# Optimization experiments

Measured on AMD Instinct MI355X. Metric: run time of the kernel, lower is better.

## Reference

```python
import jax, jax.numpy as jnp
import numpy as np

V, E, B, NODES_PER_GRAPH = 100000, 128, 4096, 64
N = B * NODES_PER_GRAPH  # 262144 nodes per side
EPS = 1e-6


def setup_inputs() -> dict:
    key = jax.random.key(0)
    k1, k2, k3, k4, k5, k6 = jax.random.split(key, 6)
    left_x = jax.random.randint(k1, (N, 1), 0, V, dtype=jnp.int64 if jax.config.jax_enable_x64 else jnp.int32)
    right_x = jax.random.randint(k2, (N, 1), 0, V, dtype=left_x.dtype)
    # sorted segment ids with every graph non-empty (64 nodes per graph)
    batch_ids = jnp.repeat(jnp.arange(B, dtype=left_x.dtype), NODES_PER_GRAPH)
    label = jax.random.randint(k3, (B,), 0, 2).astype(jnp.float32)
    emb_table = jax.random.normal(k4, (V, E), dtype=jnp.float32)
    W = jax.random.normal(k5, (E, E), dtype=jnp.float32) / np.sqrt(E)
    b = jax.random.normal(k6, (E,), dtype=jnp.float32) * 0.01
    return {
        "left_x": left_x,
        "left_graph_index": jnp.arange(B, dtype=left_x.dtype),
        "right_x": right_x,
        "right_graph_index": jnp.arange(B, dtype=left_x.dtype),
        "left_x_batch": batch_ids,
        "right_x_batch": batch_ids,
        "label": label,
        "emb_table": emb_table,
        "W": W,
        "b": b,
    }


def _side_emb(x, x_batch, emb_table, W, b, num_segments):
    node_emb = emb_table[x[:, 0]]                       # [N, E] gather
    pooled = jax.ops.segment_max(node_emb, x_batch,      # [B, E] scatter-max
                                 num_segments=num_segments,
                                 indices_are_sorted=True)
    return pooled @ W.T + b                              # trans_linear


def reference(left_x, left_graph_index, right_x, right_graph_index,
              left_x_batch, right_x_batch, label, emb_table, W, b):
    num_segments = label.shape[0]
    left_final = _side_emb(left_x, left_x_batch, emb_table, W, b, num_segments)
    right_final = _side_emb(right_x, right_x_batch, emb_table, W, b, num_segments)
    # torch CosineSimilarity(eps=1e-6): clamp each norm at eps
    dot = jnp.sum(left_final * right_final, axis=-1)
    nl = jnp.maximum(jnp.linalg.norm(left_final, axis=-1), EPS)
    nr = jnp.maximum(jnp.linalg.norm(right_final, axis=-1), EPS)
    cos = dot / (nl * nr)                                # [B]
    # ContrastiveLoss(margin=1.0), size_average=True
    losses = 0.5 * ((1.0 - label) * cos ** 2
                    + label * jnp.maximum(1.0 - cos, 0.0) ** 2)
    sim_loss = losses.mean()
    return sim_loss, cos
```

## Files before the change

kernel.cpp:

```cpp
#include <hip/hip_runtime.h>
#include <math.h>

#define B_GRAPHS 4096
#define NPG 64
#define E_DIM 128
#define INV_B (1.0f / 4096.0f)

static __device__ __forceinline__ float4 fmax4(float4 a, float4 b) {
    return make_float4(fmaxf(a.x, b.x), fmaxf(a.y, b.y),
                       fmaxf(a.z, b.z), fmaxf(a.w, b.w));
}

__global__ __launch_bounds__(256, 6) void fused_graph_sim_k(
    const int* __restrict__ lx, const int* __restrict__ rx,
    const float* __restrict__ emb, const float* __restrict__ W,
    const float* __restrict__ bias, const float* __restrict__ label,
    float* __restrict__ out)
{
    const int g    = blockIdx.x;
    const int t    = threadIdx.x;
    const int w    = t >> 6;
    const int lane = t & 63;

    __shared__ int   idxL[NPG], idxR[NPG];
    __shared__ float red[2][4][E_DIM];
    __shared__ float4 P4[2][32];
    __shared__ float wred[3][4];

    if (t < NPG)          idxL[t]       = lx[g * NPG + t];
    else if (t < 2 * NPG) idxR[t - NPG] = rx[g * NPG + (t - NPG)];
    __syncthreads();

    const int n0 = t >> 5;
    const int q  = t & 31;

    const float4* __restrict__ e4 = reinterpret_cast<const float4*>(emb);
    float4 l0 = e4[(size_t)idxL[     n0] * 32 + q];
    float4 l1 = e4[(size_t)idxL[ 8 + n0] * 32 + q];
    float4 l2 = e4[(size_t)idxL[16 + n0] * 32 + q];
    float4 l3 = e4[(size_t)idxL[24 + n0] * 32 + q];
    float4 l4 = e4[(size_t)idxL[32 + n0] * 32 + q];
    float4 l5 = e4[(size_t)idxL[40 + n0] * 32 + q];
    float4 l6 = e4[(size_t)idxL[48 + n0] * 32 + q];
    float4 l7 = e4[(size_t)idxL[56 + n0] * 32 + q];
    float4 r0 = e4[(size_t)idxR[     n0] * 32 + q];
    float4 r1 = e4[(size_t)idxR[ 8 + n0] * 32 + q];
    float4 r2 = e4[(size_t)idxR[16 + n0] * 32 + q];
    float4 r3 = e4[(size_t)idxR[24 + n0] * 32 + q];
    float4 r4 = e4[(size_t)idxR[32 + n0] * 32 + q];
    float4 r5 = e4[(size_t)idxR[40 + n0] * 32 + q];
    float4 r6 = e4[(size_t)idxR[48 + n0] * 32 + q];
    float4 r7 = e4[(size_t)idxR[56 + n0] * 32 + q];

    float4 aL = fmax4(fmax4(fmax4(l0, l1), fmax4(l2, l3)),
                      fmax4(fmax4(l4, l5), fmax4(l6, l7)));
    float4 aR = fmax4(fmax4(fmax4(r0, r1), fmax4(r2, r3)),
                      fmax4(fmax4(r4, r5), fmax4(r6, r7)));

    aL.x = fmaxf(aL.x, __shfl_xor(aL.x, 32));
    aL.y = fmaxf(aL.y, __shfl_xor(aL.y, 32));
    aL.z = fmaxf(aL.z, __shfl_xor(aL.z, 32));
    aL.w = fmaxf(aL.w, __shfl_xor(aL.w, 32));
    aR.x = fmaxf(aR.x, __shfl_xor(aR.x, 32));
    aR.y = fmaxf(aR.y, __shfl_xor(aR.y, 32));
    aR.z = fmaxf(aR.z, __shfl_xor(aR.z, 32));
    aR.w = fmaxf(aR.w, __shfl_xor(aR.w, 32));

    if (lane < 32) {
        const int o = w * 32 + lane;
        red[0][0][o] = aL.x; red[0][1][o] = aL.y;
        red[0][2][o] = aL.z; red[0][3][o] = aL.w;
        red[1][0][o] = aR.x; red[1][1][o] = aR.y;
        red[1][2][o] = aR.z; red[1][3][o] = aR.w;
    }
    __syncthreads();

    if (t < 64) {
        const int side = t >> 5;
        const int qq   = t & 31;
        float4 m;
        m.x = fmaxf(fmaxf(red[side][0][qq],      red[side][0][32 + qq]),
                    fmaxf(red[side][0][64 + qq], red[side][0][96 + qq]));
        m.y = fmaxf(fmaxf(red[side][1][qq],      red[side][1][32 + qq]),
                    fmaxf(red[side][1][64 + qq], red[side][1][96 + qq]));
        m.z = fmaxf(fmaxf(red[side][2][qq],      red[side][2][32 + qq]),
                    fmaxf(red[side][2][64 + qq], red[side][2][96 + qq]));
        m.w = fmaxf(fmaxf(red[side][3][qq],      red[side][3][32 + qq]),
                    fmaxf(red[side][3][64 + qq], red[side][3][96 + qq]));
        P4[side][qq] = m;
    }
    __syncthreads();

    float acc;
    {
        const int side = t & 1;
        const int e    = t >> 1;
        acc = bias[e];
        const float4* __restrict__ wr =
            reinterpret_cast<const float4*>(W) + (size_t)e * 32;
        const float4* __restrict__ pv = P4[side];
        #pragma unroll 8
        for (int fi = 0; fi < 32; ++fi) {
            const float4 wv = wr[fi];
            const float4 p  = pv[fi];
            acc = fmaf(p.x, wv.x, acc);
            acc = fmaf(p.y, wv.y, acc);
            acc = fmaf(p.z, wv.z, acc);
            acc = fmaf(p.w, wv.w, acc);
        }
    }

    {
        const float other = __shfl_xor(acc, 1);
        const float l = (t & 1) ? other : acc;
        const float r = (t & 1) ? acc   : other;
        float dot = l * r;
        float nl  = l * l;
        float nr  = r * r;
        #pragma unroll
        for (int off = 1; off < 64; off <<= 1) {
            dot += __shfl_xor(dot, off);
            nl  += __shfl_xor(nl,  off);
            nr  += __shfl_xor(nr,  off);
        }
        if (lane == 0) {
            wred[0][w] = dot; wred[1][w] = nl; wred[2][w] = nr;
        }
    }
    __syncthreads();

    if (t == 0) {
        const float dd = 0.5f * (wred[0][0] + wred[0][1] + wred[0][2] + wred[0][3]);
        const float ll = 0.5f * (wred[1][0] + wred[1][1] + wred[1][2] + wred[1][3]);
        const float rr = 0.5f * (wred[2][0] + wred[2][1] + wred[2][2] + wred[2][3]);
        const float nlv = fmaxf(sqrtf(ll), 1e-6f);
        const float nrv = fmaxf(sqrtf(rr), 1e-6f);
        const float c   = dd / (nlv * nrv);
        out[1 + g] = c;
        const float lab = label[g];
        const float mm  = fmaxf(1.0f - c, 0.0f);
        const float loss = 0.5f * ((1.0f - lab) * c * c + lab * mm * mm);
        atomicAdd(out, loss * INV_B);
    }
}

extern "C" void kernel_launch(void* const* d_in, const int* in_sizes, int n_in,
                              void* d_out, int out_size, void* d_ws, size_t ws_size,
                              hipStream_t stream)
{
    const int*   lx    = (const int*)d_in[0];
    const int*   rx    = (const int*)d_in[2];
    const float* label = (const float*)d_in[6];
    const float* emb   = (const float*)d_in[7];
    const float* W     = (const float*)d_in[8];
    const float* bias  = (const float*)d_in[9];

    float* out = (float*)d_out;

    hipMemsetAsync(out, 0, sizeof(float), stream);

    fused_graph_sim_k<<<B_GRAPHS, 256, 0, stream>>>(
        lx, rx, emb, W, bias, label, out);
}
```

Before: 165.2 us.

## Gather embedding rows directly into LDS via global_load_lds per side

Replaces the 16 register-held float4 gathers per thread with direct global-to-LDS loads into a 64x128 shared buffer, processing the left and right sides sequentially with a full vmcnt wait and barriers between them. The max reduction then reads the rows back from LDS. It also drops the occupancy hint from launch bounds. The intent is to cut register pressure and use the async LDS load path. The cost is that the two sides no longer overlap their loads, there are extra barriers, and a 32KB LDS footprint that may limit blocks per CU.

```diff
diff --git a/kernel.cpp b/kernel.cpp
--- a/kernel.cpp
+++ b/kernel.cpp
@@ -11,7 +11,7 @@
                        fmaxf(a.z, b.z), fmaxf(a.w, b.w));
 }
 
-__global__ __launch_bounds__(256, 6) void fused_graph_sim_k(
+__global__ __launch_bounds__(256) void fused_graph_sim_k(
     const int* __restrict__ lx, const int* __restrict__ rx,
     const float* __restrict__ emb, const float* __restrict__ W,
     const float* __restrict__ bias, const float* __restrict__ label,
@@ -22,74 +22,52 @@
     const int w    = t >> 6;
     const int lane = t & 63;
 
-    __shared__ int   idxL[NPG], idxR[NPG];
-    __shared__ float red[2][4][E_DIM];
+    __shared__ int    idxs[2][NPG];
+    __shared__ float  rows[NPG][E_DIM];
+    __shared__ float4 part[4][32];
     __shared__ float4 P4[2][32];
-    __shared__ float wred[3][4];
+    __shared__ float  wred[3][4];
 
-    if (t < NPG)          idxL[t]       = lx[g * NPG + t];
-    else if (t < 2 * NPG) idxR[t - NPG] = rx[g * NPG + (t - NPG)];
+    if (t < NPG)          idxs[0][t]       = lx[g * NPG + t];
+    else if (t < 2 * NPG) idxs[1][t - NPG] = rx[g * NPG + (t - NPG)];
     __syncthreads();
 
-    const int n0 = t >> 5;
-    const int q  = t & 31;
+    const int q     = lane & 31;
+    const int rbase = w * 16;
 
-    const float4* __restrict__ e4 = reinterpret_cast<const float4*>(emb);
-    float4 l0 = e4[(size_t)idxL[     n0] * 32 + q];
-    float4 l1 = e4[(size_t)idxL[ 8 + n0] * 32 + q];
-    float4 l2 = e4[(size_t)idxL[16 + n0] * 32 + q];
-    float4 l3 = e4[(size_t)idxL[24 + n0] * 32 + q];
-    float4 l4 = e4[(size_t)idxL[32 + n0] * 32 + q];
-    float4 l5 = e4[(size_t)idxL[40 + n0] * 32 + q];
-    float4 l6 = e4[(size_t)idxL[48 + n0] * 32 + q];
-    float4 l7 = e4[(size_t)idxL[56 + n0] * 32 + q];
-    float4 r0 = e4[(size_t)idxR[     n0] * 32 + q];
-    float4 r1 = e4[(size_t)idxR[ 8 + n0] * 32 + q];
-    float4 r2 = e4[(size_t)idxR[16 + n0] * 32 + q];
-    float4 r3 = e4[(size_t)idxR[24 + n0] * 32 + q];
-    float4 r4 = e4[(size_t)idxR[32 + n0] * 32 + q];
-    float4 r5 = e4[(size_t)idxR[40 + n0] * 32 + q];
-    float4 r6 = e4[(size_t)idxR[48 + n0] * 32 + q];
-    float4 r7 = e4[(size_t)idxR[56 + n0] * 32 + q];
+    #pragma unroll
+    for (int side = 0; side < 2; ++side) {
+        #pragma unroll
+        for (int j = 0; j < 8; ++j) {
+            const int r = rbase + 2 * j + (lane >> 5);
+            const float* gsrc =
+                emb + (size_t)idxs[side][r] * E_DIM + q * 4;
+            __builtin_amdgcn_global_load_lds(
+                (const __attribute__((address_space(1))) void*)gsrc,
+                (__attribute__((address_space(3))) void*)&rows[rbase + 2 * j][0],
+                16, 0, 0);
+        }
+        asm volatile("s_waitcnt vmcnt(0)" ::: "memory");
+        __syncthreads();
 
-    float4 aL = fmax4(fmax4(fmax4(l0, l1), fmax4(l2, l3)),
-                      fmax4(fmax4(l4, l5), fmax4(l6, l7)));
-    float4 aR = fmax4(fmax4(fmax4(r0, r1), fmax4(r2, r3)),
-                      fmax4(fmax4(r4, r5), fmax4(r6, r7)));
+        float4 m = make_float4(-INFINITY, -INFINITY, -INFINITY, -INFINITY);
+        #pragma unroll
+        for (int k = 0; k < 8; ++k) {
+            const int r = rbase + 2 * k + (lane >> 5);
+            m = fmax4(m, *reinterpret_cast<const float4*>(&rows[r][q * 4]));
+        }
+        m.x = fmaxf(m.x, __shfl_xor(m.x, 32));
+        m.y = fmaxf(m.y, __shfl_xor(m.y, 32));
+        m.z = fmaxf(m.z, __shfl_xor(m.z, 32));
+        m.w = fmaxf(m.w, __shfl_xor(m.w, 32));
+        if (lane < 32) part[w][q] = m;
+        __syncthreads();
 
-    aL.x = fmaxf(aL.x, __shfl_xor(aL.x, 32));
-    aL.y = fmaxf(aL.y, __shfl_xor(aL.y, 32));
-    aL.z = fmaxf(aL.z, __shfl_xor(aL.z, 32));
-    aL.w = fmaxf(aL.w, __shfl_xor(aL.w, 32));
-    aR.x = fmaxf(aR.x, __shfl_xor(aR.x, 32));
-    aR.y = fmaxf(aR.y, __shfl_xor(aR.y, 32));
-    aR.z = fmaxf(aR.z, __shfl_xor(aR.z, 32));
-    aR.w = fmaxf(aR.w, __shfl_xor(aR.w, 32));
-
-    if (lane < 32) {
-        const int o = w * 32 + lane;
-        red[0][0][o] = aL.x; red[0][1][o] = aL.y;
-        red[0][2][o] = aL.z; red[0][3][o] = aL.w;
-        red[1][0][o] = aR.x; red[1][1][o] = aR.y;
-        red[1][2][o] = aR.z; red[1][3][o] = aR.w;
+        if (t < 32)
+            P4[side][t] = fmax4(fmax4(part[0][t], part[1][t]),
+                                fmax4(part[2][t], part[3][t]));
+        __syncthreads();
     }
-    __syncthreads();
-
-    if (t < 64) {
-        const int side = t >> 5;
-        const int qq   = t & 31;
-        float4 m;
-        m.x = fmaxf(fmaxf(red[side][0][qq],      red[side][0][32 + qq]),
-                    fmaxf(red[side][0][64 + qq], red[side][0][96 + qq]));
-        m.y = fmaxf(fmaxf(red[side][1][qq],      red[side][1][32 + qq]),
-                    fmaxf(red[side][1][64 + qq], red[side][1][96 + qq]));
-        m.z = fmaxf(fmaxf(red[side][2][qq],      red[side][2][32 + qq]),
-                    fmaxf(red[side][2][64 + qq], red[side][2][96 + qq]));
-        m.w = fmaxf(fmaxf(red[side][3][qq],      red[side][3][32 + qq]),
-                    fmaxf(red[side][3][64 + qq], red[side][3][96 + qq]));
-        P4[side][qq] = m;
-    }
-    __syncthreads();
 
     float acc;
     {
@@ -137,8 +115,8 @@
         const float nrv = fmaxf(sqrtf(rr), 1e-6f);
         const float c   = dd / (nlv * nrv);
         out[1 + g] = c;
-        const float lab = label[g];
-        const float mm  = fmaxf(1.0f - c, 0.0f);
+        const float lab  = label[g];
+        const float mm   = fmaxf(1.0f - c, 0.0f);
         const float loss = 0.5f * ((1.0f - lab) * c * c + lab * mm * mm);
         atomicAdd(out, loss * INV_B);
     }
```

New measurement: 164.5 us. No clear change (-0.4%).
